# Performance work log

Hardware: AMD Instinct MI355X
Metric: run time of the kernel (lower is better)

## Reference

```python
import jax, jax.numpy as jnp
import numpy as np
from functools import partial

T, B, V, E, H = 512, 64, 256, 256, 512  # seq, batch, vocab, embed, lstm_hidden


def _lstm_dir(x_proj, W_hh, h0, c0):
    # x_proj: [T, B, 4H] (input projection + bias precomputed); scan only the recurrent matmul
    def step(carry, xp):
        h, c = carry
        gates = xp + h @ W_hh.T                       # [B, 4H]
        i, f, g, o = jnp.split(gates, 4, axis=-1)     # PyTorch gate order i,f,g,o
        i = jax.nn.sigmoid(i); f = jax.nn.sigmoid(f)
        g = jnp.tanh(g); o = jax.nn.sigmoid(o)
        c = f * c + i * g
        h = o * jnp.tanh(c)
        return (h, c), h
    _, hs = jax.lax.scan(step, (h0, c0), x_proj)
    return hs  # [T, B, H]


def setup_inputs() -> dict:
    key = jax.random.key(0)
    ks = jax.random.split(key, 10)
    u = lambda k, shape, s: jax.random.uniform(k, shape, jnp.float32, -s, s)
    bound = 1.0 / np.sqrt(H)
    return {
        "tokens": jax.random.randint(ks[0], (T, B), 0, V, dtype=jnp.int32),
        "h0": jnp.zeros((2, B, H), jnp.float32),
        "c0": jnp.zeros((2, B, H), jnp.float32),
        "embed_table": jax.random.normal(ks[1], (V, E), jnp.float32),
        "W_ih_f": u(ks[2], (4 * H, E), bound),
        "W_hh_f": u(ks[3], (4 * H, H), bound),
        "b_f": u(ks[4], (4 * H,), bound),   # b_ih + b_hh fused
        "W_ih_b": u(ks[5], (4 * H, E), bound),
        "W_hh_b": u(ks[6], (4 * H, H), bound),
        "b_b": u(ks[7], (4 * H,), bound),
        "W_W": u(ks[8], (2 * H, 2 * H), 0.1),
        "b_att": jnp.zeros((2 * H,), jnp.float32),  # bias_char [2H,1] squeezed; uninit in torch
        "w_proj": u(ks[9], (2 * H,), 0.1),           # weight_proj_char [2H,1] squeezed
    }


def reference(tokens, h0, c0, embed_table, W_ih_f, W_hh_f, b_f,
              W_ih_b, W_hh_b, b_b, W_W, b_att, w_proj):
    embedded = embed_table[tokens]                           # [T, B, E]
    # forward direction
    xp_f = jnp.einsum('tbe,ge->tbg', embedded, W_ih_f) + b_f
    out_f = _lstm_dir(xp_f, W_hh_f, h0[0], c0[0])            # [T, B, H]
    # backward direction (reverse time)
    xp_b = jnp.einsum('tbe,ge->tbg', embedded[::-1], W_ih_b) + b_b
    out_b = _lstm_dir(xp_b, W_hh_b, h0[1], c0[1])[::-1]      # [T, B, H]
    output = jnp.concatenate([out_f, out_b], axis=-1)        # [T, B, 2H]
    # additive attention: tanh(out @ W_W + b) . w_proj, softmax over T
    squish = jnp.tanh(jnp.einsum('tbh,hk->tbk', output, W_W) + b_att)
    scores = jnp.einsum('tbk,k->tb', squish, w_proj)         # [T, B]
    attn = jax.nn.softmax(scores, axis=0)                    # softmax over time
    char_vectors = jnp.einsum('tb,tbh->bh', attn, output)    # [B, 2H]
    return char_vectors
```

## Files before the change

kernel.cpp:

```cpp
#include <hip/hip_runtime.h>

#define T_   512
#define B_   64
#define V_   256
#define E_   256
#define H_   512
#define NWGD 32
#define THR  256

typedef _Float16 f16;
typedef _Float16 f16x8 __attribute__((ext_vector_type(8)));
typedef _Float16 f16x4 __attribute__((ext_vector_type(4)));
typedef float    f32x4 __attribute__((ext_vector_type(4)));

#define WS_CTL      0
#define WS_CTL_END  8192
#define WS_SCORES   WS_CTL_END
#define WS_ATTN     (WS_SCORES + 512*64*4)
#define WS_ZERO_END (WS_ATTN + 512*64*4)
#define WS_TAB      WS_ZERO_END
#define WS_WARR     (WS_TAB + 256*256*2)
#define WS_WWT      (WS_WARR + 2*2048*768*2)
#define WS_HBUF     (WS_WWT + 1024*1024*2)
#define WS_OUT      (WS_HBUF + 2*2*64*512*2)
#define WS_END      (WS_OUT + (size_t)512*64*1024*2)

__device__ inline int load_int_sc1(const int* p) {
    int v;
    asm volatile("global_load_dword %0, %1, off sc1\n\ts_waitcnt vmcnt(0)"
                 : "=v"(v) : "v"(p) : "memory");
    return v;
}

__device__ inline void store_int_sc1(int* p, int v) {
    asm volatile("global_store_dword %0, %1, off sc1"
                 :: "v"(p), "v"(v) : "memory");
}

__device__ inline void store_f16x4_sc1(f16* p, f16x4 v) {
    asm volatile("global_store_dwordx2 %0, %1, off sc1"
                 :: "v"(p), "v"(v) : "memory");
}

__device__ inline void drain_vm() {
    asm volatile("s_waitcnt vmcnt(0)" ::: "memory");
}

#define LD4(dst, base, OFFB) \
    asm volatile("global_load_dwordx4 %0, %1, off offset:" #OFFB \
                 : "=v"(dst) : "v"(base))
#define LD4S(dst, base, OFFB) \
    asm volatile("global_load_dwordx4 %0, %1, off offset:" #OFFB " sc1" \
                 : "=v"(dst) : "v"(base))
#define WAITVM(N) do { \
    asm volatile("s_waitcnt vmcnt(" #N ")" ::: "memory"); \
    __builtin_amdgcn_sched_barrier(0); } while (0)

__global__ void k_setup_table(const float* __restrict__ et, f16* __restrict__ tab) {
    int i = blockIdx.x * 256 + threadIdx.x;
    tab[i] = (f16)et[i];
}

__global__ void k_setup_wwt(const float* __restrict__ ww, f16* __restrict__ wwt) {
    int i = blockIdx.x * 256 + threadIdx.x;
    int col = i >> 10, h = i & 1023;
    wwt[(col << 10) + h] = (f16)ww[(h << 10) + col];
}

__global__ void k_setup_warr(const float* __restrict__ wihf, const float* __restrict__ whhf,
                             const float* __restrict__ wihb, const float* __restrict__ whhb,
                             f16* __restrict__ warr) {
    int i = blockIdx.x * 256 + threadIdx.x;
    int k = i % 768;
    int r = i / 768;
    int colp = r & 63;
    int wg   = (r >> 6) & 31;
    int dir  = r >> 11;
    int gate = colp >> 4, u = colp & 15;
    int row = gate * 512 + wg * 16 + u;
    const float* wih = dir ? wihb : wihf;
    const float* whh = dir ? whhb : whhf;
    float v = (k < 256) ? wih[row * 256 + k] : whh[row * 512 + (k - 256)];
    warr[i] = (f16)v;
}

#define GSTR 68

__launch_bounds__(THR, 1)
__global__ void k_lstm(const int* __restrict__ tokens,
                       const float* __restrict__ h0, const float* __restrict__ c0,
                       const float* __restrict__ b_f, const float* __restrict__ b_b,
                       const f16* __restrict__ tab, const f16* __restrict__ warr,
                       f16* __restrict__ hbuf, f16* __restrict__ outcat,
                       int* __restrict__ ctl) {
    __shared__ float gate[64 * GSTR];
    __shared__ float cst[64 * 16];

    const int tid = threadIdx.x;
    const int dir = blockIdx.x >> 5, wg = blockIdx.x & 31;
    int* flags = ctl + 64 + dir * 512;

    const int l = tid & 63, w = tid >> 6;
    const int mh = w >> 1, nh = w & 1;
    const int r0 = mh * 32 + (l & 15), r1 = r0 + 16;
    const int kofs = (l >> 4) * 8;

    f16x8 bf0[24], bf1[24];
#pragma unroll
    for (int kt = 0; kt < 24; ++kt) {
        int colp0 = nh * 32 + 0 * 16 + (l & 15);
        int colp1 = nh * 32 + 1 * 16 + (l & 15);
        long base = (long)((dir * 32 + wg) * 64) * 768;
        bf0[kt] = *(const f16x8*)(warr + base + (long)colp0 * 768 + kt * 32 + kofs);
        bf1[kt] = *(const f16x8*)(warr + base + (long)colp1 * 768 + kt * 32 + kofs);
    }

    const int pb = tid >> 2;
    const int u0 = (tid & 3) * 4;
    const float* bv = dir ? b_b : b_f;
    f32x4 bias[4];
#pragma unroll
    for (int g = 0; g < 4; ++g)
        bias[g] = *(const f32x4*)(bv + g * 512 + wg * 16 + u0);

    {
        f32x4 cv = *(const f32x4*)(c0 + (dir * 64 + pb) * 512 + wg * 16 + u0);
        *(f32x4*)(cst + pb * 16 + u0) = cv;
        f32x4 h4 = *(const f32x4*)(h0 + (dir * 64 + pb) * 512 + wg * 16 + u0);
        f16x4 hv;
#pragma unroll
        for (int j = 0; j < 4; ++j) hv[j] = (f16)h4[j];
        store_f16x4_sc1(hbuf + ((0 * 2 + dir) * 64 + pb) * 512 + wg * 16 + u0, hv);
    }
    drain_vm();
    __syncthreads();
    if (tid == 0) store_int_sc1(flags + wg * 16, 1);

    int tok0 = tokens[(dir ? 511 : 0) * 64 + r0];
    int tok1 = tokens[(dir ? 511 : 0) * 64 + r1];

#pragma unroll 1
    for (int s = 0; s < 512; ++s) {
        const int t_act = dir ? (511 - s) : s;

        f16x8 e0[8], e1[8];
        {
            const f16* p0 = tab + tok0 * 256 + kofs;
            const f16* p1 = tab + tok1 * 256 + kofs;
            LD4(e0[0], p0, 0);   LD4(e1[0], p1, 0);
            LD4(e0[1], p0, 64);  LD4(e1[1], p1, 64);
            LD4(e0[2], p0, 128); LD4(e1[2], p1, 128);
            LD4(e0[3], p0, 192); LD4(e1[3], p1, 192);
            LD4(e0[4], p0, 256); LD4(e1[4], p1, 256);
            LD4(e0[5], p0, 320); LD4(e1[5], p1, 320);
            LD4(e0[6], p0, 384); LD4(e1[6], p1, 384);
            LD4(e0[7], p0, 448); LD4(e1[7], p1, 448);
        }

        {
            const int* fp = flags + (l & 31) * 16;
            const int target = s + 1;
            int guard = 0;
            while (true) {
                int v = load_int_sc1(fp);
                if (__all(v >= target)) break;
                if (++guard > 8192) break;
            }
        }
        __builtin_amdgcn_sched_barrier(0);

        const f16* hbase = hbuf + (long)(((s & 1) * 2 + dir) * 64) * 512;
        const f16* pr0 = hbase + r0 * 512 + kofs;
        const f16* pr1 = hbase + r1 * 512 + kofs;
        f16x8 ha0[8], ha1[8], hc0[8], hc1[8];
        LD4S(ha0[0], pr0, 0);   LD4S(ha1[0], pr1, 0);
        LD4S(ha0[1], pr0, 64);  LD4S(ha1[1], pr1, 64);
        LD4S(ha0[2], pr0, 128); LD4S(ha1[2], pr1, 128);
        LD4S(ha0[3], pr0, 192); LD4S(ha1[3], pr1, 192);
        LD4S(ha0[4], pr0, 256); LD4S(ha1[4], pr1, 256);
        LD4S(ha0[5], pr0, 320); LD4S(ha1[5], pr1, 320);
        LD4S(ha0[6], pr0, 384); LD4S(ha1[6], pr1, 384);
        LD4S(ha0[7], pr0, 448); LD4S(ha1[7], pr1, 448);

        f32x4 a00 = {0.f,0.f,0.f,0.f}, a01 = {0.f,0.f,0.f,0.f};
        f32x4 a10 = {0.f,0.f,0.f,0.f}, a11 = {0.f,0.f,0.f,0.f};
#pragma unroll
        for (int kt = 0; kt < 8; ++kt) {
            a00 = __builtin_amdgcn_mfma_f32_16x16x32_f16(e0[kt], bf0[kt], a00, 0, 0, 0);
            a01 = __builtin_amdgcn_mfma_f32_16x16x32_f16(e0[kt], bf1[kt], a01, 0, 0, 0);
            a10 = __builtin_amdgcn_mfma_f32_16x16x32_f16(e1[kt], bf0[kt], a10, 0, 0, 0);
            a11 = __builtin_amdgcn_mfma_f32_16x16x32_f16(e1[kt], bf1[kt], a11, 0, 0, 0);
        }

        LD4S(hc0[0], pr0, 512); LD4S(hc1[0], pr1, 512);
        LD4S(hc0[1], pr0, 576); LD4S(hc1[1], pr1, 576);
        LD4S(hc0[2], pr0, 640); LD4S(hc1[2], pr1, 640);
        LD4S(hc0[3], pr0, 704); LD4S(hc1[3], pr1, 704);
        LD4S(hc0[4], pr0, 768); LD4S(hc1[4], pr1, 768);
        LD4S(hc0[5], pr0, 832); LD4S(hc1[5], pr1, 832);
        LD4S(hc0[6], pr0, 896); LD4S(hc1[6], pr1, 896);
        LD4S(hc0[7], pr0, 960); LD4S(hc1[7], pr1, 960);

        WAITVM(16);
#pragma unroll
        for (int kt = 0; kt < 8; ++kt) {
            a00 = __builtin_amdgcn_mfma_f32_16x16x32_f16(ha0[kt], bf0[kt + 8], a00, 0, 0, 0);
            a01 = __builtin_amdgcn_mfma_f32_16x16x32_f16(ha0[kt], bf1[kt + 8], a01, 0, 0, 0);
            a10 = __builtin_amdgcn_mfma_f32_16x16x32_f16(ha1[kt], bf0[kt + 8], a10, 0, 0, 0);
            a11 = __builtin_amdgcn_mfma_f32_16x16x32_f16(ha1[kt], bf1[kt + 8], a11, 0, 0, 0);
        }
        WAITVM(0);
#pragma unroll
        for (int kt = 0; kt < 8; ++kt) {
            a00 = __builtin_amdgcn_mfma_f32_16x16x32_f16(hc0[kt], bf0[kt + 16], a00, 0, 0, 0);
            a01 = __builtin_amdgcn_mfma_f32_16x16x32_f16(hc0[kt], bf1[kt + 16], a01, 0, 0, 0);
            a10 = __builtin_amdgcn_mfma_f32_16x16x32_f16(hc1[kt], bf0[kt + 16], a10, 0, 0, 0);
            a11 = __builtin_amdgcn_mfma_f32_16x16x32_f16(hc1[kt], bf1[kt + 16], a11, 0, 0, 0);
        }

#pragma unroll
        for (int q = 0; q < 4; ++q) {
            int br0 = mh * 32 + (l >> 4) * 4 + q;
            int br1 = br0 + 16;
            int cl0 = nh * 32 + (l & 15);
            gate[br0 * GSTR + cl0]      = a00[q];
            gate[br0 * GSTR + cl0 + 16] = a01[q];
            gate[br1 * GSTR + cl0]      = a10[q];
            gate[br1 * GSTR + cl0 + 16] = a11[q];
        }
        __syncthreads();

        {
            int sn = (s < 511) ? (s + 1) : 511;
            int tn = dir ? (511 - sn) : sn;
            tok0 = tokens[tn * 64 + r0];
            tok1 = tokens[tn * 64 + r1];
        }
        {
            f32x4 g0 = *(const f32x4*)(gate + pb * GSTR +  0 + u0);
            f32x4 g1 = *(const f32x4*)(gate + pb * GSTR + 16 + u0);
            f32x4 g2 = *(const f32x4*)(gate + pb * GSTR + 32 + u0);
            f32x4 g3 = *(const f32x4*)(gate + pb * GSTR + 48 + u0);
            f32x4 cv = *(const f32x4*)(cst + pb * 16 + u0);
            f16x4 hv;
#pragma unroll
            for (int j = 0; j < 4; ++j) {
                float gi = g0[j] + bias[0][j];
                float gf = g1[j] + bias[1][j];
                float gg = g2[j] + bias[2][j];
                float go = g3[j] + bias[3][j];
                float si = 1.f / (1.f + __expf(-gi));
                float sf = 1.f / (1.f + __expf(-gf));
                float tg = tanhf(gg);
                float so = 1.f / (1.f + __expf(-go));
                float c = sf * cv[j] + si * tg;
                float h = so * tanhf(c);
                cv[j] = c;
                hv[j] = (f16)h;
            }
            *(f32x4*)(cst + pb * 16 + u0) = cv;
            store_f16x4_sc1(hbuf + ((((s + 1) & 1) * 2 + dir) * 64 + pb) * 512 + wg * 16 + u0, hv);
            *(f16x4*)(outcat + ((long)t_act * 64 + pb) * 1024 + dir * 512 + wg * 16 + u0) = hv;
        }
        drain_vm();
        __syncthreads();
        if (tid == 0) store_int_sc1(flags + wg * 16, s + 2);
    }
}

__global__ void k_attn_gemm(const f16* __restrict__ outcat, const f16* __restrict__ wwt,
                            const float* __restrict__ b_att, const float* __restrict__ w_proj,
                            float* __restrict__ scores) {
    __shared__ __align__(16) f16 A2[64][136];
    __shared__ __align__(16) f16 B2[64][136];
    __shared__ float sq[64][68];
    const int tid = threadIdx.x;
    const int mb = blockIdx.x >> 4, nb = blockIdx.x & 15;
    const int r0 = mb * 64, c0 = nb * 64;
    const int l = tid & 63, w = tid >> 6;
    const int mh = w >> 1, nhf = w & 1;

    f32x4 acc[2][2];
#pragma unroll
    for (int m = 0; m < 2; ++m)
#pragma unroll
        for (int n = 0; n < 2; ++n)
            acc[m][n] = (f32x4){0.f, 0.f, 0.f, 0.f};

    for (int kc = 0; kc < 8; ++kc) {
        int k0 = kc * 128;
        {
            int row = tid >> 2, seg = tid & 3;
            const f16* sa = outcat + (long)(r0 + row) * 1024 + k0 + seg * 32;
            const f16* sb = wwt + (long)(c0 + row) * 1024 + k0 + seg * 32;
#pragma unroll
            for (int j = 0; j < 4; ++j) {
                *(f16x8*)(&A2[row][seg * 32 + j * 8]) = *(const f16x8*)(sa + j * 8);
                *(f16x8*)(&B2[row][seg * 32 + j * 8]) = *(const f16x8*)(sb + j * 8);
            }
        }
        __syncthreads();
        const int kofs = (l >> 4) * 8;
#pragma unroll
        for (int kt = 0; kt < 4; ++kt) {
            int ko = kt * 32 + kofs;
            f16x8 a0 = *(const f16x8*)(&A2[mh * 32 + (l & 15)][ko]);
            f16x8 a1 = *(const f16x8*)(&A2[mh * 32 + 16 + (l & 15)][ko]);
            f16x8 b0 = *(const f16x8*)(&B2[nhf * 32 + (l & 15)][ko]);
            f16x8 b1 = *(const f16x8*)(&B2[nhf * 32 + 16 + (l & 15)][ko]);
            acc[0][0] = __builtin_amdgcn_mfma_f32_16x16x32_f16(a0, b0, acc[0][0], 0, 0, 0);
            acc[0][1] = __builtin_amdgcn_mfma_f32_16x16x32_f16(a0, b1, acc[0][1], 0, 0, 0);
            acc[1][0] = __builtin_amdgcn_mfma_f32_16x16x32_f16(a1, b0, acc[1][0], 0, 0, 0);
            acc[1][1] = __builtin_amdgcn_mfma_f32_16x16x32_f16(a1, b1, acc[1][1], 0, 0, 0);
        }
        __syncthreads();
    }
#pragma unroll
    for (int m = 0; m < 2; ++m)
#pragma unroll
        for (int n = 0; n < 2; ++n)
#pragma unroll
            for (int q = 0; q < 4; ++q) {
                int rl = mh * 32 + m * 16 + (l >> 4) * 4 + q;
                int cl = nhf * 32 + n * 16 + (l & 15);
                int cg = c0 + cl;
                sq[rl][cl] = tanhf(acc[m][n][q] + b_att[cg]) * w_proj[cg];
            }
    __syncthreads();
    if (tid < 64) {
        float s = 0.f;
#pragma unroll
        for (int c2 = 0; c2 < 64; ++c2) s += sq[tid][c2];
        atomicAdd(scores + r0 + tid, s);
    }
}

__global__ void k_softmax(const float* __restrict__ scores, float* __restrict__ attn) {
    const int b = blockIdx.x, tid = threadIdx.x;
    __shared__ float redm[4];
    __shared__ float reds[4];
    float v0 = scores[(tid * 2 + 0) * 64 + b];
    float v1 = scores[(tid * 2 + 1) * 64 + b];
    float m = fmaxf(v0, v1);
#pragma unroll
    for (int off = 32; off; off >>= 1) m = fmaxf(m, __shfl_down(m, off));
    if ((tid & 63) == 0) redm[tid >> 6] = m;
    __syncthreads();
    m = fmaxf(fmaxf(redm[0], redm[1]), fmaxf(redm[2], redm[3]));
    float e0 = __expf(v0 - m), e1 = __expf(v1 - m);
    float s = e0 + e1;
#pragma unroll
    for (int off = 32; off; off >>= 1) s += __shfl_down(s, off);
    if ((tid & 63) == 0) reds[tid >> 6] = s;
    __syncthreads();
    s = (reds[0] + reds[1]) + (reds[2] + reds[3]);
    float inv = 1.f / s;
    attn[(tid * 2 + 0) * 64 + b] = e0 * inv;
    attn[(tid * 2 + 1) * 64 + b] = e1 * inv;
}

__global__ void k_wsum(const float* __restrict__ attn, const f16* __restrict__ outcat,
                       float* __restrict__ out) {
    const int b = blockIdx.x, tid = threadIdx.x;
    float a0 = 0.f, a1 = 0.f, a2 = 0.f, a3 = 0.f;
    for (int t = 0; t < 512; ++t) {
        float at = attn[t * 64 + b];
        f16x4 v = *(const f16x4*)(outcat + ((long)t * 64 + b) * 1024 + tid * 4);
        a0 += at * (float)v[0];
        a1 += at * (float)v[1];
        a2 += at * (float)v[2];
        a3 += at * (float)v[3];
    }
    float* dst = out + b * 1024 + tid * 4;
    dst[0] = a0; dst[1] = a1; dst[2] = a2; dst[3] = a3;
}

extern "C" void kernel_launch(void* const* d_in, const int* in_sizes, int n_in,
                              void* d_out, int out_size, void* d_ws, size_t ws_size,
                              hipStream_t stream) {
    if (ws_size < WS_END) return;

    const int*   tokens = (const int*)d_in[0];
    const float* h0     = (const float*)d_in[1];
    const float* c0     = (const float*)d_in[2];
    const float* etab   = (const float*)d_in[3];
    const float* wihf   = (const float*)d_in[4];
    const float* whhf   = (const float*)d_in[5];
    const float* b_f    = (const float*)d_in[6];
    const float* wihb   = (const float*)d_in[7];
    const float* whhb   = (const float*)d_in[8];
    const float* b_b    = (const float*)d_in[9];
    const float* ww     = (const float*)d_in[10];
    const float* b_att  = (const float*)d_in[11];
    const float* w_proj = (const float*)d_in[12];
    float* out = (float*)d_out;

    char* ws = (char*)d_ws;
    int*   ctl    = (int*)(ws + WS_CTL);
    float* scores = (float*)(ws + WS_SCORES);
    float* attn   = (float*)(ws + WS_ATTN);
    f16*   tab    = (f16*)(ws + WS_TAB);
    f16*   warr   = (f16*)(ws + WS_WARR);
    f16*   wwt    = (f16*)(ws + WS_WWT);
    f16*   hbuf   = (f16*)(ws + WS_HBUF);
    f16*   outcat = (f16*)(ws + WS_OUT);

    hipMemsetAsync(d_ws, 0, WS_ZERO_END, stream);

    k_setup_table<<<256, 256, 0, stream>>>(etab, tab);
    k_setup_wwt<<<4096, 256, 0, stream>>>(ww, wwt);
    k_setup_warr<<<12288, 256, 0, stream>>>(wihf, whhf, wihb, whhb, warr);

    k_lstm<<<64, THR, 0, stream>>>(tokens, h0, c0, b_f, b_b,
                                   tab, warr, hbuf, outcat, ctl);

    k_attn_gemm<<<8192, 256, 0, stream>>>(outcat, wwt, b_att, w_proj, scores);
    k_softmax<<<64, 256, 0, stream>>>(scores, attn);
    k_wsum<<<64, 256, 0, stream>>>(attn, outcat, out);
}
```

Before: 4.376 ms.

## Use per-wave readiness flags in LSTM recurrence and drop end-of-step barrier

Replaces the per-workgroup step flag, which needed a __syncthreads before thread 0 published it, with one flag per wave. Each lane now polls only the flags of the waves that produced the batch rows it consumes. The workgroup barrier at the end of each step is removed, the outcat store is moved after the flag publish, and s_sleep is added in the poll loop. tanhf is replaced with an exp-based fast tanh. The aim is to shorten the serial critical path per timestep. The cost is more flags to poll, a different exp-based tanh approximation, and reliance on finer-grained ordering between waves.

Measured after the change: 4.329 ms. About the same (-1.1%).

```diff
diff --git a/kernel.cpp b/kernel.cpp
--- a/kernel.cpp
+++ b/kernel.cpp
@@ -14,7 +14,7 @@
 typedef float    f32x4 __attribute__((ext_vector_type(4)));
 
 #define WS_CTL      0
-#define WS_CTL_END  8192
+#define WS_CTL_END  20480
 #define WS_SCORES   WS_CTL_END
 #define WS_ATTN     (WS_SCORES + 512*64*4)
 #define WS_ZERO_END (WS_ATTN + 512*64*4)
@@ -55,6 +55,14 @@
 #define WAITVM(N) do { \
     asm volatile("s_waitcnt vmcnt(" #N ")" ::: "memory"); \
     __builtin_amdgcn_sched_barrier(0); } while (0)
+
+__device__ inline float fast_sigmoid(float x) {
+    return 1.f / (1.f + __expf(-x));
+}
+__device__ inline float fast_tanh(float x) {
+    float e = __expf(-2.f * x);
+    return 2.f / (1.f + e) - 1.f;
+}
 
 __global__ void k_setup_table(const float* __restrict__ et, f16* __restrict__ tab) {
     int i = blockIdx.x * 256 + threadIdx.x;
@@ -98,12 +106,14 @@
 
     const int tid = threadIdx.x;
     const int dir = blockIdx.x >> 5, wg = blockIdx.x & 31;
-    int* flags = ctl + 64 + dir * 512;
 
     const int l = tid & 63, w = tid >> 6;
     const int mh = w >> 1, nh = w & 1;
     const int r0 = mh * 32 + (l & 15), r1 = r0 + 16;
     const int kofs = (l >> 4) * 8;
+
+    int* myflag = ctl + 64 + ((dir * 32 + wg) * 4 + w) * 16;
+    const int* pollp = ctl + 64 + ((dir * 32 + (l >> 1)) * 4 + mh * 2 + (l & 1)) * 16;
 
     f16x8 bf0[24], bf1[24];
 #pragma unroll
@@ -133,8 +143,8 @@
         store_f16x4_sc1(hbuf + ((0 * 2 + dir) * 64 + pb) * 512 + wg * 16 + u0, hv);
     }
     drain_vm();
+    if ((tid & 63) == 0) store_int_sc1(myflag, 1);
     __syncthreads();
-    if (tid == 0) store_int_sc1(flags + wg * 16, 1);
 
     int tok0 = tokens[(dir ? 511 : 0) * 64 + r0];
     int tok1 = tokens[(dir ? 511 : 0) * 64 + r1];
@@ -158,13 +168,13 @@
         }
 
         {
-            const int* fp = flags + (l & 31) * 16;
             const int target = s + 1;
             int guard = 0;
             while (true) {
-                int v = load_int_sc1(fp);
+                int v = load_int_sc1(pollp);
                 if (__all(v >= target)) break;
-                if (++guard > 8192) break;
+                __builtin_amdgcn_s_sleep(1);
+                if (++guard > 4096) break;
             }
         }
         __builtin_amdgcn_sched_barrier(0);
@@ -236,35 +246,30 @@
             tok0 = tokens[tn * 64 + r0];
             tok1 = tokens[tn * 64 + r1];
         }
+        f16x4 hv;
         {
             f32x4 g0 = *(const f32x4*)(gate + pb * GSTR +  0 + u0);
             f32x4 g1 = *(const f32x4*)(gate + pb * GSTR + 16 + u0);
             f32x4 g2 = *(const f32x4*)(gate + pb * GSTR + 32 + u0);
             f32x4 g3 = *(const f32x4*)(gate + pb * GSTR + 48 + u0);
             f32x4 cv = *(const f32x4*)(cst + pb * 16 + u0);
-            f16x4 hv;
 #pragma unroll
             for (int j = 0; j < 4; ++j) {
-                float gi = g0[j] + bias[0][j];
-                float gf = g1[j] + bias[1][j];
-                float gg = g2[j] + bias[2][j];
-                float go = g3[j] + bias[3][j];
-                float si = 1.f / (1.f + __expf(-gi));
-                float sf = 1.f / (1.f + __expf(-gf));
-                float tg = tanhf(gg);
-                float so = 1.f / (1.f + __expf(-go));
+                float si = fast_sigmoid(g0[j] + bias[0][j]);
+                float sf = fast_sigmoid(g1[j] + bias[1][j]);
+                float tg = fast_tanh(g2[j] + bias[2][j]);
+                float so = fast_sigmoid(g3[j] + bias[3][j]);
                 float c = sf * cv[j] + si * tg;
-                float h = so * tanhf(c);
+                float h = so * fast_tanh(c);
                 cv[j] = c;
                 hv[j] = (f16)h;
             }
             *(f32x4*)(cst + pb * 16 + u0) = cv;
             store_f16x4_sc1(hbuf + ((((s + 1) & 1) * 2 + dir) * 64 + pb) * 512 + wg * 16 + u0, hv);
-            *(f16x4*)(outcat + ((long)t_act * 64 + pb) * 1024 + dir * 512 + wg * 16 + u0) = hv;
         }
         drain_vm();
-        __syncthreads();
-        if (tid == 0) store_int_sc1(flags + wg * 16, s + 2);
+        if ((tid & 63) == 0) store_int_sc1(myflag, s + 2);
+        *(f16x4*)(outcat + ((long)t_act * 64 + pb) * 1024 + dir * 512 + wg * 16 + u0) = hv;
     }
 }
 
```
